# Kernel optimization log

Measured on AMD Instinct MI355X. Metric: run time of the kernel, lower is better.

The kernel has to match this reference:

```python
import jax, jax.numpy as jnp
import numpy as np

N = 50000        # nodes
E_RND = 800000   # random edges (self-loops appended -> E = 850000)
IN = 256         # in_dim
H1, D = 4, 32    # heads[0], num_hidden
C = 40           # num_classes (heads[1] = 1)
SLOPE = 0.2      # leaky_relu negative_slope
EPS = 1e-5       # batchnorm eps


def setup_inputs() -> dict:
    key = jax.random.key(0)
    ks = jax.random.split(key, 9)
    x = jax.random.normal(ks[0], (N, IN), jnp.float32)
    loops = jnp.arange(N, dtype=jnp.int32)
    src = jnp.concatenate([jax.random.randint(ks[1], (E_RND,), 0, N, dtype=jnp.int32), loops])
    dst = jnp.concatenate([jax.random.randint(ks[2], (E_RND,), 0, N, dtype=jnp.int32), loops])
    glorot = lambda k, shape, fan: jax.random.normal(k, shape, jnp.float32) * np.float32(1.0 / np.sqrt(fan))
    W1 = glorot(ks[3], (IN, H1 * D), IN)
    al1 = glorot(ks[4], (H1, D), D)
    ar1 = glorot(ks[5], (H1, D), D)
    gamma = jnp.ones((H1 * D,), jnp.float32)
    beta = jnp.zeros((H1 * D,), jnp.float32)
    W2 = glorot(ks[6], (H1 * D, C), H1 * D)
    al2 = glorot(ks[7], (1, C), C)
    ar2 = glorot(ks[8], (1, C), C)
    return dict(x=x, src=src, dst=dst, W1=W1, al1=al1, ar1=ar1,
                gamma=gamma, beta=beta, W2=W2, al2=al2, ar2=ar2)


def _gat_conv(h, src, dst, W, al, ar, heads, out_dim):
    """DGL GATConv (eval mode: dropouts are identity, no residual/bias)."""
    n = h.shape[0]
    ft = (h @ W).reshape(n, heads, out_dim)              # (N,H,D)
    el = jnp.einsum('nhd,hd->nh', ft, al)                # (N,H)
    er = jnp.einsum('nhd,hd->nh', ft, ar)
    e = jax.nn.leaky_relu(el[src] + er[dst], SLOPE)      # (E,H)
    # edge softmax over incoming edges per destination node (stable)
    m = jax.ops.segment_max(e, dst, num_segments=n)
    m = jnp.where(jnp.isfinite(m), m, 0.0)
    ex = jnp.exp(e - m[dst])
    s = jax.ops.segment_sum(ex, dst, num_segments=n)
    a = ex / jnp.maximum(s[dst], 1e-9)                   # (E,H)
    msg = a[:, :, None] * ft[src]                        # (E,H,D)
    return jax.ops.segment_sum(msg, dst, num_segments=n) # (N,H,D)


def reference(x, src, dst, W1, al1, ar1, gamma, beta, W2, al2, ar2):
    h = _gat_conv(x, src, dst, W1, al1, ar1, H1, D).reshape(N, H1 * D)
    mu = jnp.mean(h, axis=0)
    var = jnp.var(h, axis=0)                              # biased var, as torch BN training
    h = (h - mu) * jax.lax.rsqrt(var + EPS) * gamma + beta
    h = jax.nn.elu(h)
    logits = _gat_conv(h, src, dst, W2, al2, ar2, 1, C).mean(axis=1)  # (N,C)
    return jax.nn.log_softmax(logits, axis=-1)
```

## Files before the change

kernel.cpp:

```cpp
#include <hip/hip_runtime.h>
#include <hip/hip_bf16.h>
#include <math.h>

#define N_NODES 50000
#define N_EDGES 850000
#define IN_DIM  256
#define HD      128
#define H1      4
#define D       32
#define NC      40
#define SLOPE   0.2f
#define EPS_BN  1e-5f

#define NBIN    782
#define BCAP    1536
#define NREP    32
#define RCAP    128
#define NWAVE   4

typedef __attribute__((ext_vector_type(8))) short bf16x8;
typedef __attribute__((ext_vector_type(4))) float f32x4;
typedef unsigned long long u64;

__device__ __forceinline__ unsigned short f2bf(float x) {
    union { float f; unsigned u; } v; v.f = x;
    unsigned r = v.u + 0x7FFF + ((v.u >> 16) & 1);
    return (unsigned short)(r >> 16);
}
__device__ __forceinline__ float bf2f(unsigned short h) {
    union { unsigned u; float f; } v; v.u = ((unsigned)h) << 16;
    return v.f;
}
__device__ __forceinline__ uint4 pack8(float a0,float a1,float a2,float a3,
                                       float a4,float a5,float a6,float a7) {
    uint4 p;
    p.x = f2bf(a0) | ((unsigned)f2bf(a1) << 16);
    p.y = f2bf(a2) | ((unsigned)f2bf(a3) << 16);
    p.z = f2bf(a4) | ((unsigned)f2bf(a5) << 16);
    p.w = f2bf(a6) | ((unsigned)f2bf(a7) << 16);
    return p;
}

__device__ __forceinline__ int tile32_addr(int row, int chunk) {
    return row * 32 + ((chunk ^ ((row >> 1) & 3)) << 3);
}

__global__ __launch_bounds__(256) void binscatter_k(const int* __restrict__ src,
                                                    const int* __restrict__ dst,
                                                    int* __restrict__ bincur,
                                                    unsigned* __restrict__ tmp,
                                                    const float* __restrict__ W1,
                                                    const float* __restrict__ W2,
                                                    unsigned short* __restrict__ W1t,
                                                    unsigned short* __restrict__ W2t) {
    int e = blockIdx.x * blockDim.x + threadIdx.x;
    if (e < IN_DIM * HD) {
        int k = e >> 7, n = e & 127;
        W1t[n * IN_DIM + k] = f2bf(W1[e]);
    }
    if (e < 48 * HD) {
        int n = e >> 7, k = e & 127;
        float v = (n < NC) ? W2[k * NC + n] : 0.f;
        W2t[e] = f2bf(v);
    }
    if (e >= N_EDGES) return;
    int v = dst[e];
    int b = v >> 6;
    int rep = e & (NREP - 1);
    int cell = b * NREP + rep;
    int cur = atomicAdd(&bincur[cell], 1);
    if (cur < RCAP)
        tmp[(size_t)cell * RCAP + cur] = ((unsigned)(v & 63) << 16) | (unsigned)src[e];
}

__global__ __launch_bounds__(256) void binsort_k(const unsigned* __restrict__ tmp,
                                                 const int* __restrict__ bincur,
                                                 unsigned* __restrict__ csrp,
                                                 u64* __restrict__ rowp,
                                                 int* __restrict__ bintot) {
    __shared__ int cnts[NREP];
    __shared__ int hist[64];
    __shared__ int cur[64];
    int b = blockIdx.x, tid = threadIdx.x;
    int nbase = b << 6;
    size_t cbase = (size_t)b * BCAP;
    int wv = tid >> 6, ln = tid & 63;
    if (tid < NREP) cnts[tid] = min(bincur[b * NREP + tid], RCAP);
    if (tid < 64) hist[tid] = 0;
    __syncthreads();
    for (int s = wv; s < NREP; s += NWAVE) {
        int c = cnts[s];
        const unsigned* seg = tmp + (size_t)(b * NREP + s) * RCAP;
        for (int t = ln; t < c; t += 64)
            atomicAdd(&hist[seg[t] >> 16], 1);
    }
    __syncthreads();
    if (tid < 64) {
        int h = hist[tid];
        int v = h;
        #pragma unroll
        for (int off = 1; off < 64; off <<= 1) {
            int t2 = __shfl_up(v, off);
            if (tid >= off) v += t2;
        }
        int excl = v - h;
        cur[tid] = excl;
        int node = nbase + tid;
        if (node < N_NODES)
            rowp[node] = ((u64)h << 32) | (unsigned)(cbase + excl);
        if (tid == 63) bintot[b] = v;
    }
    __syncthreads();
    for (int s = wv; s < NREP; s += NWAVE) {
        int c = cnts[s];
        const unsigned* seg = tmp + (size_t)(b * NREP + s) * RCAP;
        for (int t = ln; t < c; t += 64) {
            unsigned p = seg[t];
            int pos = atomicAdd(&cur[p >> 16], 1);
            csrp[cbase + pos] = p;
        }
    }
}

__global__ __launch_bounds__(256) void mfma1_k(const float* __restrict__ X,
                                               const unsigned short* __restrict__ W1t,
                                               unsigned short* __restrict__ ftb) {
    __shared__ unsigned short alds[2][64 * 32];
    __shared__ unsigned short wlds[2][128 * 32];
    const int tid = threadIdx.x;
    const int lane = tid & 63, wid = tid >> 6;
    const int wr = wid >> 1, wc = wid & 1;
    const int rowBase = blockIdx.x * 64;
    const int s_arow = tid >> 2, s_ac = tid & 3;
    const int s_wcol = tid >> 1, s_wc0 = (tid & 1) * 2;

    auto stageA = [&](int buf, int ks) {
        float4 v0 = make_float4(0.f,0.f,0.f,0.f), v1 = v0;
        int gr = rowBase + s_arow;
        if (gr < N_NODES) {
            const float4* p = (const float4*)(X + (size_t)gr * IN_DIM + ks * 32 + s_ac * 8);
            v0 = p[0]; v1 = p[1];
        }
        *(uint4*)&alds[buf][tile32_addr(s_arow, s_ac)] =
            pack8(v0.x,v0.y,v0.z,v0.w,v1.x,v1.y,v1.z,v1.w);
    };
    auto stageW = [&](int buf, int ks) {
        const uint4* g = (const uint4*)(W1t + s_wcol * IN_DIM + ks * 32 + s_wc0 * 8);
        uint4 a = g[0], b = g[1];
        *(uint4*)&wlds[buf][tile32_addr(s_wcol, s_wc0)] = a;
        *(uint4*)&wlds[buf][tile32_addr(s_wcol, s_wc0 + 1)] = b;
    };

    f32x4 acc[2][4];
    #pragma unroll
    for (int mf = 0; mf < 2; ++mf)
        #pragma unroll
        for (int nf = 0; nf < 4; ++nf)
            acc[mf][nf] = (f32x4){0.f, 0.f, 0.f, 0.f};

    stageA(0, 0); stageW(0, 0);
    for (int ks = 0; ks < 8; ++ks) {
        __syncthreads();
        if (ks < 7) { stageA((ks + 1) & 1, ks + 1); stageW((ks + 1) & 1, ks + 1); }
        int buf = ks & 1;
        bf16x8 afrag[2], bfrag[4];
        #pragma unroll
        for (int mf = 0; mf < 2; ++mf) {
            int row = wr * 32 + mf * 16 + (lane & 15);
            afrag[mf] = *(const bf16x8*)&alds[buf][tile32_addr(row, lane >> 4)];
        }
        #pragma unroll
        for (int nf = 0; nf < 4; ++nf) {
            int col = wc * 64 + nf * 16 + (lane & 15);
            bfrag[nf] = *(const bf16x8*)&wlds[buf][tile32_addr(col, lane >> 4)];
        }
        #pragma unroll
        for (int mf = 0; mf < 2; ++mf)
            #pragma unroll
            for (int nf = 0; nf < 4; ++nf)
                acc[mf][nf] = __builtin_amdgcn_mfma_f32_16x16x32_bf16(
                    afrag[mf], bfrag[nf], acc[mf][nf], 0, 0, 0);
    }
    #pragma unroll
    for (int mf = 0; mf < 2; ++mf) {
        int r0 = rowBase + wr * 32 + mf * 16 + (lane >> 4) * 4;
        #pragma unroll
        for (int nf = 0; nf < 4; ++nf) {
            int col = wc * 64 + nf * 16 + (lane & 15);
            #pragma unroll
            for (int v = 0; v < 4; ++v) {
                int r = r0 + v;
                if (r < N_NODES) ftb[(size_t)r * HD + col] = f2bf(acc[mf][nf][v]);
            }
        }
    }
}

__global__ __launch_bounds__(256) void mfma2_k(const unsigned short* __restrict__ Hin,
                                               const unsigned short* __restrict__ W2t,
                                               const float* __restrict__ bnsum,
                                               const float* __restrict__ bnsq,
                                               const float* __restrict__ gamma,
                                               const float* __restrict__ beta,
                                               unsigned short* __restrict__ ft2b) {
    __shared__ unsigned short alds[2][64 * 32];
    __shared__ unsigned short wlds[48 * 128];
    __shared__ float sc_lds[HD], sh_lds[HD];
    const int tid = threadIdx.x;
    const int lane = tid & 63, wid = tid >> 6;
    const int rowBase = blockIdx.x * 64;
    const int s_arow = tid >> 2, s_ac = tid & 3;

    if (tid < HD) {
        const float invN = 1.0f / (float)N_NODES;
        float mu = bnsum[tid] * invN;
        float var = bnsq[tid] * invN - mu * mu;
        float sc = gamma[tid] * rsqrtf(var + EPS_BN);
        sc_lds[tid] = sc;
        sh_lds[tid] = beta[tid] - mu * sc;
    }
    for (int i = tid; i < 48 * 16; i += 256) {
        int col = i >> 4, c = i & 15;
        uint4 v = *(const uint4*)(W2t + col * HD + c * 8);
        *(uint4*)&wlds[col * HD + ((c ^ (col & 7)) << 3)] = v;
    }
    __syncthreads();

    auto stageA = [&](int buf, int ks) {
        int c0 = ks * 32 + s_ac * 8;
        uint4 pv = make_uint4(0,0,0,0);
        int gr = rowBase + s_arow;
        if (gr < N_NODES) pv = *(const uint4*)(Hin + (size_t)gr * HD + c0);
        float4 sc0 = *(const float4*)(sc_lds + c0), sc1 = *(const float4*)(sc_lds + c0 + 4);
        float4 sh0 = *(const float4*)(sh_lds + c0), sh1 = *(const float4*)(sh_lds + c0 + 4);
        float t[8];
        t[0] = fmaf(bf2f(pv.x & 0xffff), sc0.x, sh0.x);
        t[1] = fmaf(bf2f(pv.x >> 16),    sc0.y, sh0.y);
        t[2] = fmaf(bf2f(pv.y & 0xffff), sc0.z, sh0.z);
        t[3] = fmaf(bf2f(pv.y >> 16),    sc0.w, sh0.w);
        t[4] = fmaf(bf2f(pv.z & 0xffff), sc1.x, sh1.x);
        t[5] = fmaf(bf2f(pv.z >> 16),    sc1.y, sh1.y);
        t[6] = fmaf(bf2f(pv.w & 0xffff), sc1.z, sh1.z);
        t[7] = fmaf(bf2f(pv.w >> 16),    sc1.w, sh1.w);
        #pragma unroll
        for (int i = 0; i < 8; ++i) t[i] = t[i] > 0.f ? t[i] : expm1f(t[i]);
        *(uint4*)&alds[buf][tile32_addr(s_arow, s_ac)] =
            pack8(t[0],t[1],t[2],t[3],t[4],t[5],t[6],t[7]);
    };

    f32x4 acc[3];
    #pragma unroll
    for (int nf = 0; nf < 3; ++nf) acc[nf] = (f32x4){0.f, 0.f, 0.f, 0.f};

    stageA(0, 0);
    for (int ks = 0; ks < 4; ++ks) {
        __syncthreads();
        if (ks < 3) stageA((ks + 1) & 1, ks + 1);
        int buf = ks & 1;
        int row = wid * 16 + (lane & 15);
        bf16x8 a = *(const bf16x8*)&alds[buf][tile32_addr(row, lane >> 4)];
        #pragma unroll
        for (int nf = 0; nf < 3; ++nf) {
            int col = nf * 16 + (lane & 15);
            int c = ks * 4 + (lane >> 4);
            bf16x8 b = *(const bf16x8*)&wlds[col * HD + ((c ^ (col & 7)) << 3)];
            acc[nf] = __builtin_amdgcn_mfma_f32_16x16x32_bf16(a, b, acc[nf], 0, 0, 0);
        }
    }
    int r0 = rowBase + wid * 16 + (lane >> 4) * 4;
    #pragma unroll
    for (int nf = 0; nf < 3; ++nf) {
        int col = nf * 16 + (lane & 15);
        if (col < NC) {
            #pragma unroll
            for (int v = 0; v < 4; ++v) {
                int r = r0 + v;
                if (r < N_NODES) ft2b[(size_t)r * NC + col] = f2bf(acc[nf][v]);
            }
        }
    }
}

__global__ void eler1b_k(const unsigned short* __restrict__ ftb,
                         const float* __restrict__ alw, const float* __restrict__ arw,
                         float* __restrict__ el, float* __restrict__ er) {
    int t = blockIdx.x * blockDim.x + threadIdx.x;
    if (t >= N_NODES * H1) return;
    int n = t >> 2, h = t & 3;
    const unsigned short* f = ftb + (size_t)n * HD + h * D;
    const float* a = alw + h * D;
    const float* r = arw + h * D;
    float sl = 0.f, sr = 0.f;
    #pragma unroll
    for (int d = 0; d < D; d += 8) {
        uint4 fv = *(const uint4*)(f + d);
        float x0 = bf2f(fv.x & 0xffff), x1 = bf2f(fv.x >> 16);
        float x2 = bf2f(fv.y & 0xffff), x3 = bf2f(fv.y >> 16);
        float x4 = bf2f(fv.z & 0xffff), x5 = bf2f(fv.z >> 16);
        float x6 = bf2f(fv.w & 0xffff), x7 = bf2f(fv.w >> 16);
        sl += x0*a[d] + x1*a[d+1] + x2*a[d+2] + x3*a[d+3]
            + x4*a[d+4] + x5*a[d+5] + x6*a[d+6] + x7*a[d+7];
        sr += x0*r[d] + x1*r[d+1] + x2*r[d+2] + x3*r[d+3]
            + x4*r[d+4] + x5*r[d+5] + x6*r[d+6] + x7*r[d+7];
    }
    el[t] = sl; er[t] = sr;
}

__global__ void eler2b_k(const unsigned short* __restrict__ ft2b,
                         const float* __restrict__ alw, const float* __restrict__ arw,
                         float* __restrict__ el, float* __restrict__ er) {
    int n = blockIdx.x * blockDim.x + threadIdx.x;
    if (n >= N_NODES) return;
    const unsigned short* f = ft2b + (size_t)n * NC;
    float sl = 0.f, sr = 0.f;
    #pragma unroll
    for (int d = 0; d < NC; d += 4) {
        uint2 fv = *(const uint2*)(f + d);
        float x0 = bf2f(fv.x & 0xffff), x1 = bf2f(fv.x >> 16);
        float x2 = bf2f(fv.y & 0xffff), x3 = bf2f(fv.y >> 16);
        sl += x0*alw[d] + x1*alw[d+1] + x2*alw[d+2] + x3*alw[d+3];
        sr += x0*arw[d] + x1*arw[d+1] + x2*arw[d+2] + x3*arw[d+3];
    }
    el[n] = sl; er[n] = sr;
}

__global__ void exw1_k(const unsigned* __restrict__ csrp,
                       const int* __restrict__ bintot,
                       const float* __restrict__ el, const float* __restrict__ er,
                       float4* __restrict__ exw) {
    int s = blockIdx.x * blockDim.x + threadIdx.x;
    int b = s / BCAP;
    int off = s - b * BCAP;
    if (off >= bintot[b]) return;
    unsigned p = csrp[s];
    int u = p & 0xffff;
    int v = (b << 6) + (p >> 16);
    const float4 l = *(const float4*)(el + u * H1);
    const float4 r = *(const float4*)(er + v * H1);
    float4 o;
    float t;
    t = l.x + r.x; t = t > 0.f ? t : SLOPE * t; o.x = __expf(t);
    t = l.y + r.y; t = t > 0.f ? t : SLOPE * t; o.y = __expf(t);
    t = l.z + r.z; t = t > 0.f ? t : SLOPE * t; o.z = __expf(t);
    t = l.w + r.w; t = t > 0.f ? t : SLOPE * t; o.w = __expf(t);
    exw[s] = o;
}

__global__ void exw2_k(const unsigned* __restrict__ csrp,
                       const int* __restrict__ bintot,
                       const float* __restrict__ el, const float* __restrict__ er,
                       float* __restrict__ exw) {
    int s = blockIdx.x * blockDim.x + threadIdx.x;
    int b = s / BCAP;
    int off = s - b * BCAP;
    if (off >= bintot[b]) return;
    unsigned p = csrp[s];
    float t = el[p & 0xffff] + er[(b << 6) + (p >> 16)];
    t = t > 0.f ? t : SLOPE * t;
    exw[s] = __expf(t);
}

__global__ __launch_bounds__(256) void gather1_k(const u64* __restrict__ rowp,
                                                 const unsigned* __restrict__ csrp,
                                                 const float* __restrict__ exw,
                                                 const unsigned short* __restrict__ ftb,
                                                 unsigned int* __restrict__ h1b) {
    int w = (blockIdx.x * blockDim.x + threadIdx.x) >> 6;
    if (w >= N_NODES) return;
    int lane = threadIdx.x & 63;
    int hh = lane >> 4;
    u64 rp = rowp[w];
    int jb = (int)(rp & 0xffffffffu), je = jb + (int)(rp >> 32);
    float ax = 0.f, ay = 0.f, ssum = 0.f;
    int j = jb;
    for (; j + 3 < je; j += 4) {
        int u0 = csrp[j] & 0xffff, u1 = csrp[j+1] & 0xffff;
        int u2 = csrp[j+2] & 0xffff, u3 = csrp[j+3] & 0xffff;
        float w0 = exw[(size_t)j*H1 + hh];
        float w1 = exw[(size_t)(j+1)*H1 + hh];
        float w2 = exw[(size_t)(j+2)*H1 + hh];
        float w3 = exw[(size_t)(j+3)*H1 + hh];
        ushort2 f0 = *(const ushort2*)(ftb + (size_t)u0 * HD + lane * 2);
        ushort2 f1 = *(const ushort2*)(ftb + (size_t)u1 * HD + lane * 2);
        ushort2 f2 = *(const ushort2*)(ftb + (size_t)u2 * HD + lane * 2);
        ushort2 f3 = *(const ushort2*)(ftb + (size_t)u3 * HD + lane * 2);
        ax = fmaf(w0, bf2f(f0.x), ax); ay = fmaf(w0, bf2f(f0.y), ay);
        ax = fmaf(w1, bf2f(f1.x), ax); ay = fmaf(w1, bf2f(f1.y), ay);
        ax = fmaf(w2, bf2f(f2.x), ax); ay = fmaf(w2, bf2f(f2.y), ay);
        ax = fmaf(w3, bf2f(f3.x), ax); ay = fmaf(w3, bf2f(f3.y), ay);
        ssum += (w0 + w1) + (w2 + w3);
    }
    for (; j < je; ++j) {
        int u0 = csrp[j] & 0xffff;
        float w0 = exw[(size_t)j*H1 + hh];
        ushort2 f0 = *(const ushort2*)(ftb + (size_t)u0 * HD + lane * 2);
        ax = fmaf(w0, bf2f(f0.x), ax); ay = fmaf(w0, bf2f(f0.y), ay);
        ssum += w0;
    }
    float inv = 1.0f / fmaxf(ssum, 1e-9f);
    h1b[(size_t)w * 64 + lane] = (unsigned)f2bf(ax * inv)
                               | ((unsigned)f2bf(ay * inv) << 16);
}

__global__ void bnstats_k(const unsigned short* __restrict__ h1b,
                          float* __restrict__ sums, float* __restrict__ sumsq) {
    int c = threadIdx.x;
    float acc = 0.f, acc2 = 0.f;
    for (int r = blockIdx.x; r < N_NODES; r += gridDim.x) {
        float v = bf2f(h1b[(size_t)r * HD + c]);
        acc += v; acc2 += v * v;
    }
    atomicAdd(&sums[c], acc);
    atomicAdd(&sumsq[c], acc2);
}

__global__ __launch_bounds__(256) void gather2_k(const u64* __restrict__ rowp,
                                                 const unsigned* __restrict__ csrp,
                                                 const float* __restrict__ exw,
                                                 const unsigned short* __restrict__ ft2b,
                                                 float* __restrict__ out) {
    int w = (blockIdx.x * blockDim.x + threadIdx.x) >> 6;
    if (w >= N_NODES) return;
    int lane = threadIdx.x & 63;
    u64 rp = rowp[w];
    int jb = (int)(rp & 0xffffffffu), je = jb + (int)(rp >> 32);
    float acc = 0.f, ssum = 0.f;
    int j = jb;
    for (; j + 3 < je; j += 4) {
        int u0 = csrp[j] & 0xffff, u1 = csrp[j+1] & 0xffff;
        int u2 = csrp[j+2] & 0xffff, u3 = csrp[j+3] & 0xffff;
        float w0 = exw[j], w1 = exw[j+1], w2 = exw[j+2], w3 = exw[j+3];
        float fa = (lane < NC) ? bf2f(ft2b[(size_t)u0 * NC + lane]) : 0.f;
        float fb = (lane < NC) ? bf2f(ft2b[(size_t)u1 * NC + lane]) : 0.f;
        float fc = (lane < NC) ? bf2f(ft2b[(size_t)u2 * NC + lane]) : 0.f;
        float fd = (lane < NC) ? bf2f(ft2b[(size_t)u3 * NC + lane]) : 0.f;
        acc = fmaf(w0, fa, acc); acc = fmaf(w1, fb, acc);
        acc = fmaf(w2, fc, acc); acc = fmaf(w3, fd, acc);
        ssum += (w0 + w1) + (w2 + w3);
    }
    for (; j < je; ++j) {
        int u0 = csrp[j] & 0xffff;
        float w0 = exw[j];
        float fa = (lane < NC) ? bf2f(ft2b[(size_t)u0 * NC + lane]) : 0.f;
        acc = fmaf(w0, fa, acc);
        ssum += w0;
    }
    float v = acc / fmaxf(ssum, 1e-9f);
    float vv = (lane < NC) ? v : -INFINITY;
    float m = vv;
    #pragma unroll
    for (int off = 32; off; off >>= 1) m = fmaxf(m, __shfl_xor(m, off));
    float ex2 = (lane < NC) ? __expf(vv - m) : 0.f;
    float sum = ex2;
    #pragma unroll
    for (int off = 32; off; off >>= 1) sum += __shfl_xor(sum, off);
    if (lane < NC) out[(size_t)w * NC + lane] = vv - m - logf(sum);
}

extern "C" void kernel_launch(void* const* d_in, const int* in_sizes, int n_in,
                              void* d_out, int out_size, void* d_ws, size_t ws_size,
                              hipStream_t stream) {
    const float* x     = (const float*)d_in[0];
    const int*   src   = (const int*)  d_in[1];
    const int*   dst   = (const int*)  d_in[2];
    const float* W1    = (const float*)d_in[3];
    const float* al1   = (const float*)d_in[4];
    const float* ar1   = (const float*)d_in[5];
    const float* gamma = (const float*)d_in[6];
    const float* beta  = (const float*)d_in[7];
    const float* W2    = (const float*)d_in[8];
    const float* al2   = (const float*)d_in[9];
    const float* ar2   = (const float*)d_in[10];
    float* out = (float*)d_out;

    const size_t NSLOT = (size_t)NBIN * BCAP;
    const size_t NTMP  = (size_t)NBIN * NREP * RCAP;

    char* ws = (char*)d_ws;
    size_t o = 0;
    auto allocB = [&](size_t bytes) { void* p = ws + o; o += (bytes + 15) & ~15ull; return p; };
    int*   bincur = (int*)allocB((size_t)NBIN * NREP * 4);
    float* bnsum  = (float*)allocB(HD * 4);
    float* bnsq   = (float*)allocB(HD * 4);
    size_t zeroBytes = o;
    unsigned* tmp  = (unsigned*)allocB(NTMP * 4);
    unsigned* csrp = (unsigned*)allocB(NSLOT * 4);
    int*   bintot  = (int*)allocB(NBIN * 4);
    u64*   rowp    = (u64*)allocB((size_t)N_NODES * 8);
    float4* exw1   = (float4*)allocB(NSLOT * 16);
    float*  exw2   = (float*)allocB(NSLOT * 4);
    unsigned short* w1t  = (unsigned short*)allocB((size_t)IN_DIM * HD * 2);
    unsigned short* w2t  = (unsigned short*)allocB((size_t)48 * HD * 2);
    unsigned short* ft1b = (unsigned short*)allocB((size_t)N_NODES * HD * 2);
    unsigned int*   h1b  = (unsigned int*)allocB((size_t)N_NODES * HD * 2);
    float* el1  = (float*)allocB(N_NODES * H1 * 4);
    float* er1  = (float*)allocB(N_NODES * H1 * 4);
    unsigned short* ft2b = (unsigned short*)allocB((size_t)N_NODES * NC * 2);
    float* el2  = (float*)allocB(N_NODES * 4);
    float* er2  = (float*)allocB(N_NODES * 4);

    hipMemsetAsync(d_ws, 0, zeroBytes, stream);

    const int NB_E = (N_EDGES + 255) / 256;
    const int NB_G = (N_NODES + 63) / 64;
    const int NB_S = (int)(NSLOT / 256);

    binscatter_k<<<NB_E, 256, 0, stream>>>(src, dst, bincur, tmp, W1, W2, w1t, w2t);
    binsort_k<<<NBIN, 256, 0, stream>>>(tmp, bincur, csrp, rowp, bintot);

    mfma1_k<<<NB_G, 256, 0, stream>>>(x, w1t, ft1b);
    eler1b_k<<<(N_NODES * H1 + 255) / 256, 256, 0, stream>>>(ft1b, al1, ar1, el1, er1);
    exw1_k<<<NB_S, 256, 0, stream>>>(csrp, bintot, el1, er1, exw1);
    gather1_k<<<N_NODES / 4, 256, 0, stream>>>(rowp, csrp, (const float*)exw1, ft1b, h1b);

    bnstats_k<<<512, HD, 0, stream>>>((const unsigned short*)h1b, bnsum, bnsq);

    mfma2_k<<<NB_G, 256, 0, stream>>>((const unsigned short*)h1b, w2t,
                                      bnsum, bnsq, gamma, beta, ft2b);
    eler2b_k<<<(N_NODES + 255) / 256, 256, 0, stream>>>(ft2b, al2, ar2, el2, er2);
    exw2_k<<<NB_S, 256, 0, stream>>>(csrp, bintot, el2, er2, exw2);
    gather2_k<<<N_NODES / 4, 256, 0, stream>>>(rowp, csrp, exw2, ft2b, out);
}
```

Measured before the change: 352.8 us.

## Fuse edge attention-weight computation into gather kernels and unroll by eight

Drops the separate exw1/exw2 kernels that materialized per-edge exp weights into large workspace buffers. The gather kernels now compute leaky_relu and exp on the fly from el[src] and a per-destination er value loaded once. The main loop is also unrolled from four to eight edges to keep more loads in flight. This removes two launches and the write-then-read of the weight arrays. In exchange it adds redundant exp work across lanes and extra random reads of el per edge.

```diff
diff --git a/kernel.cpp b/kernel.cpp
--- a/kernel.cpp
+++ b/kernel.cpp
@@ -324,75 +324,46 @@
     el[n] = sl; er[n] = sr;
 }
 
-__global__ void exw1_k(const unsigned* __restrict__ csrp,
-                       const int* __restrict__ bintot,
-                       const float* __restrict__ el, const float* __restrict__ er,
-                       float4* __restrict__ exw) {
-    int s = blockIdx.x * blockDim.x + threadIdx.x;
-    int b = s / BCAP;
-    int off = s - b * BCAP;
-    if (off >= bintot[b]) return;
-    unsigned p = csrp[s];
-    int u = p & 0xffff;
-    int v = (b << 6) + (p >> 16);
-    const float4 l = *(const float4*)(el + u * H1);
-    const float4 r = *(const float4*)(er + v * H1);
-    float4 o;
-    float t;
-    t = l.x + r.x; t = t > 0.f ? t : SLOPE * t; o.x = __expf(t);
-    t = l.y + r.y; t = t > 0.f ? t : SLOPE * t; o.y = __expf(t);
-    t = l.z + r.z; t = t > 0.f ? t : SLOPE * t; o.z = __expf(t);
-    t = l.w + r.w; t = t > 0.f ? t : SLOPE * t; o.w = __expf(t);
-    exw[s] = o;
-}
-
-__global__ void exw2_k(const unsigned* __restrict__ csrp,
-                       const int* __restrict__ bintot,
-                       const float* __restrict__ el, const float* __restrict__ er,
-                       float* __restrict__ exw) {
-    int s = blockIdx.x * blockDim.x + threadIdx.x;
-    int b = s / BCAP;
-    int off = s - b * BCAP;
-    if (off >= bintot[b]) return;
-    unsigned p = csrp[s];
-    float t = el[p & 0xffff] + er[(b << 6) + (p >> 16)];
-    t = t > 0.f ? t : SLOPE * t;
-    exw[s] = __expf(t);
-}
-
 __global__ __launch_bounds__(256) void gather1_k(const u64* __restrict__ rowp,
                                                  const unsigned* __restrict__ csrp,
-                                                 const float* __restrict__ exw,
+                                                 const float* __restrict__ el,
+                                                 const float* __restrict__ er,
                                                  const unsigned short* __restrict__ ftb,
                                                  unsigned int* __restrict__ h1b) {
     int w = (blockIdx.x * blockDim.x + threadIdx.x) >> 6;
     if (w >= N_NODES) return;
     int lane = threadIdx.x & 63;
     int hh = lane >> 4;
+    float erv = er[w * H1 + hh];
     u64 rp = rowp[w];
     int jb = (int)(rp & 0xffffffffu), je = jb + (int)(rp >> 32);
     float ax = 0.f, ay = 0.f, ssum = 0.f;
     int j = jb;
-    for (; j + 3 < je; j += 4) {
-        int u0 = csrp[j] & 0xffff, u1 = csrp[j+1] & 0xffff;
-        int u2 = csrp[j+2] & 0xffff, u3 = csrp[j+3] & 0xffff;
-        float w0 = exw[(size_t)j*H1 + hh];
-        float w1 = exw[(size_t)(j+1)*H1 + hh];
-        float w2 = exw[(size_t)(j+2)*H1 + hh];
-        float w3 = exw[(size_t)(j+3)*H1 + hh];
-        ushort2 f0 = *(const ushort2*)(ftb + (size_t)u0 * HD + lane * 2);
-        ushort2 f1 = *(const ushort2*)(ftb + (size_t)u1 * HD + lane * 2);
-        ushort2 f2 = *(const ushort2*)(ftb + (size_t)u2 * HD + lane * 2);
-        ushort2 f3 = *(const ushort2*)(ftb + (size_t)u3 * HD + lane * 2);
-        ax = fmaf(w0, bf2f(f0.x), ax); ay = fmaf(w0, bf2f(f0.y), ay);
-        ax = fmaf(w1, bf2f(f1.x), ax); ay = fmaf(w1, bf2f(f1.y), ay);
-        ax = fmaf(w2, bf2f(f2.x), ax); ay = fmaf(w2, bf2f(f2.y), ay);
-        ax = fmaf(w3, bf2f(f3.x), ax); ay = fmaf(w3, bf2f(f3.y), ay);
-        ssum += (w0 + w1) + (w2 + w3);
+    for (; j + 7 < je; j += 8) {
+        int u[8]; float wv[8]; ushort2 f[8];
+        #pragma unroll
+        for (int k = 0; k < 8; ++k) u[k] = csrp[j + k] & 0xffff;
+        #pragma unroll
+        for (int k = 0; k < 8; ++k)
+            f[k] = *(const ushort2*)(ftb + (size_t)u[k] * HD + lane * 2);
+        #pragma unroll
+        for (int k = 0; k < 8; ++k) {
+            float t = el[u[k] * H1 + hh] + erv;
+            t = t > 0.f ? t : SLOPE * t;
+            wv[k] = __expf(t);
+        }
+        #pragma unroll
+        for (int k = 0; k < 8; ++k) {
+            ax = fmaf(wv[k], bf2f(f[k].x), ax);
+            ay = fmaf(wv[k], bf2f(f[k].y), ay);
+            ssum += wv[k];
+        }
     }
     for (; j < je; ++j) {
         int u0 = csrp[j] & 0xffff;
-        float w0 = exw[(size_t)j*H1 + hh];
+        float t = el[u0 * H1 + hh] + erv;
+        t = t > 0.f ? t : SLOPE * t;
+        float w0 = __expf(t);
         ushort2 f0 = *(const ushort2*)(ftb + (size_t)u0 * HD + lane * 2);
         ax = fmaf(w0, bf2f(f0.x), ax); ay = fmaf(w0, bf2f(f0.y), ay);
         ssum += w0;
@@ -416,31 +387,42 @@
 
 __global__ __launch_bounds__(256) void gather2_k(const u64* __restrict__ rowp,
                                                  const unsigned* __restrict__ csrp,
-                                                 const float* __restrict__ exw,
+                                                 const float* __restrict__ el,
+                                                 const float* __restrict__ er,
                                                  const unsigned short* __restrict__ ft2b,
                                                  float* __restrict__ out) {
     int w = (blockIdx.x * blockDim.x + threadIdx.x) >> 6;
     if (w >= N_NODES) return;
     int lane = threadIdx.x & 63;
+    float erv = er[w];
     u64 rp = rowp[w];
     int jb = (int)(rp & 0xffffffffu), je = jb + (int)(rp >> 32);
     float acc = 0.f, ssum = 0.f;
     int j = jb;
-    for (; j + 3 < je; j += 4) {
-        int u0 = csrp[j] & 0xffff, u1 = csrp[j+1] & 0xffff;
-        int u2 = csrp[j+2] & 0xffff, u3 = csrp[j+3] & 0xffff;
-        float w0 = exw[j], w1 = exw[j+1], w2 = exw[j+2], w3 = exw[j+3];
-        float fa = (lane < NC) ? bf2f(ft2b[(size_t)u0 * NC + lane]) : 0.f;
-        float fb = (lane < NC) ? bf2f(ft2b[(size_t)u1 * NC + lane]) : 0.f;
-        float fc = (lane < NC) ? bf2f(ft2b[(size_t)u2 * NC + lane]) : 0.f;
-        float fd = (lane < NC) ? bf2f(ft2b[(size_t)u3 * NC + lane]) : 0.f;
-        acc = fmaf(w0, fa, acc); acc = fmaf(w1, fb, acc);
-        acc = fmaf(w2, fc, acc); acc = fmaf(w3, fd, acc);
-        ssum += (w0 + w1) + (w2 + w3);
+    for (; j + 7 < je; j += 8) {
+        int u[8]; float wv[8]; float fv[8];
+        #pragma unroll
+        for (int k = 0; k < 8; ++k) u[k] = csrp[j + k] & 0xffff;
+        #pragma unroll
+        for (int k = 0; k < 8; ++k)
+            fv[k] = (lane < NC) ? bf2f(ft2b[(size_t)u[k] * NC + lane]) : 0.f;
+        #pragma unroll
+        for (int k = 0; k < 8; ++k) {
+            float t = el[u[k]] + erv;
+            t = t > 0.f ? t : SLOPE * t;
+            wv[k] = __expf(t);
+        }
+        #pragma unroll
+        for (int k = 0; k < 8; ++k) {
+            acc = fmaf(wv[k], fv[k], acc);
+            ssum += wv[k];
+        }
     }
     for (; j < je; ++j) {
         int u0 = csrp[j] & 0xffff;
-        float w0 = exw[j];
+        float t = el[u0] + erv;
+        t = t > 0.f ? t : SLOPE * t;
+        float w0 = __expf(t);
         float fa = (lane < NC) ? bf2f(ft2b[(size_t)u0 * NC + lane]) : 0.f;
         acc = fmaf(w0, fa, acc);
         ssum += w0;
@@ -487,8 +469,6 @@
     unsigned* csrp = (unsigned*)allocB(NSLOT * 4);
     int*   bintot  = (int*)allocB(NBIN * 4);
     u64*   rowp    = (u64*)allocB((size_t)N_NODES * 8);
-    float4* exw1   = (float4*)allocB(NSLOT * 16);
-    float*  exw2   = (float*)allocB(NSLOT * 4);
     unsigned short* w1t  = (unsigned short*)allocB((size_t)IN_DIM * HD * 2);
     unsigned short* w2t  = (unsigned short*)allocB((size_t)48 * HD * 2);
     unsigned short* ft1b = (unsigned short*)allocB((size_t)N_NODES * HD * 2);
@@ -503,21 +483,18 @@
 
     const int NB_E = (N_EDGES + 255) / 256;
     const int NB_G = (N_NODES + 63) / 64;
-    const int NB_S = (int)(NSLOT / 256);
 
     binscatter_k<<<NB_E, 256, 0, stream>>>(src, dst, bincur, tmp, W1, W2, w1t, w2t);
     binsort_k<<<NBIN, 256, 0, stream>>>(tmp, bincur, csrp, rowp, bintot);
 
     mfma1_k<<<NB_G, 256, 0, stream>>>(x, w1t, ft1b);
     eler1b_k<<<(N_NODES * H1 + 255) / 256, 256, 0, stream>>>(ft1b, al1, ar1, el1, er1);
-    exw1_k<<<NB_S, 256, 0, stream>>>(csrp, bintot, el1, er1, exw1);
-    gather1_k<<<N_NODES / 4, 256, 0, stream>>>(rowp, csrp, (const float*)exw1, ft1b, h1b);
+    gather1_k<<<N_NODES / 4, 256, 0, stream>>>(rowp, csrp, el1, er1, ft1b, h1b);
 
     bnstats_k<<<512, HD, 0, stream>>>((const unsigned short*)h1b, bnsum, bnsq);
 
     mfma2_k<<<NB_G, 256, 0, stream>>>((const unsigned short*)h1b, w2t,
                                       bnsum, bnsq, gamma, beta, ft2b);
     eler2b_k<<<(N_NODES + 255) / 256, 256, 0, stream>>>(ft2b, al2, ar2, el2, er2);
-    exw2_k<<<NB_S, 256, 0, stream>>>(csrp, bintot, el2, er2, exw2);
-    gather2_k<<<N_NODES / 4, 256, 0, stream>>>(rowp, csrp, exw2, ft2b, out);
-}
+    gather2_k<<<N_NODES / 4, 256, 0, stream>>>(rowp, csrp, el2, er2, ft2b, out);
+}
```

Result: no change. 347.2 us (-1.6%).
